# Kernel optimization log

Hardware: AMD Instinct MI355X
Metric: run time of the kernel (lower is better)

## Reference

```python
import jax, jax.numpy as jnp
import numpy as np

H = 16          # num query heads
G = 4           # num kv heads (groups)
MAX_POS = 128   # max relative position


def setup_inputs() -> dict:
    key = jax.random.key(0)
    ks = jax.random.split(key, 6)
    B, T, D = 8, 1024, 1024
    hd = D // H
    s = 0.02
    return {
        "x": jax.random.normal(ks[0], (B, T, D), jnp.float32),
        "Wq": jax.random.normal(ks[1], (D, D), jnp.float32) * s,
        "Wk": jax.random.normal(ks[2], (hd * G, D), jnp.float32) * s,
        "Wv": jax.random.normal(ks[3], (hd * G, D), jnp.float32) * s,
        "Wo": jax.random.normal(ks[4], (D, D), jnp.float32) * s,
        "E": jax.random.normal(ks[5], (2 * MAX_POS - 1, hd), jnp.float32) * s,
    }


def reference(x, Wq, Wk, Wv, Wo, E):
    B, T, D = x.shape
    hd = D // H
    r = H // G  # kv repeat factor

    # projections (torch nn.Linear convention: y = x @ W.T)
    q = (x @ Wq.T).reshape(B, T, H, hd).transpose(0, 2, 1, 3)  # [B,H,T,hd]
    k = (x @ Wk.T).reshape(B, T, G, hd)                         # [B,T,G,hd]
    v = (x @ Wv.T).reshape(B, T, G, hd)

    # GQA: query head h uses kv group h // r  (matches repeat_interleave)
    k = jnp.repeat(k, r, axis=2).transpose(0, 2, 1, 3)  # [B,H,T,hd]
    v = jnp.repeat(v, r, axis=2).transpose(0, 2, 1, 3)  # [B,H,T,hd]

    q = q * (1.0 / hd) ** 0.5
    scores = jnp.einsum("bhqd,bhkd->bhqk", q, k)  # [B,H,T,T]

    # relative position bias: R[i,j] = E[clamp(j - i) + MAX_POS - 1]
    pos = jnp.arange(T)
    dist = jnp.clip(pos[None, :] - pos[:, None], -MAX_POS + 1, MAX_POS - 1) + MAX_POS - 1
    R = E[dist]  # [T,T,hd]
    # original einsum 'bhd,thd->bht' with q=[B*H, Tq, hd], R=[Tk, Tq, hd]:
    # bias[b,h,q,kpos] = sum_d q[b,h,q,d] * R[kpos, q, d]
    bias = jnp.einsum("bhqd,kqd->bhqk", q, R)
    scores = scores + bias

    attn = jax.nn.softmax(scores, axis=-1)
    out = jnp.einsum("bhqk,bhkd->bhqd", attn, v)         # [B,H,T,hd]
    out = out.transpose(0, 2, 1, 3).reshape(B, T, D)      # [B,T,D]
    return out @ Wo.T
```

## Files before the change

kernel.cpp:

```cpp
#include <hip/hip_runtime.h>
#include <hip/hip_bf16.h>
#include <cstdint>
#include <cstddef>

typedef __hip_bfloat16 bf16;
typedef __attribute__((ext_vector_type(8))) __bf16 bf16x8;
typedef __attribute__((ext_vector_type(4))) float floatx4;

#define GPTR(p) ((const __attribute__((address_space(1))) void*)(p))
#define LPTR(p) ((__attribute__((address_space(3))) void*)(p))

extern "C" __device__ float __ocml_native_exp2_f32(float);
__device__ __forceinline__ float exp2n(float x) {
  return __ocml_native_exp2_f32(x);
}

__device__ __forceinline__ floatx4 mfma16(bf16x8 a, bf16x8 b, floatx4 c) {
  return __builtin_amdgcn_mfma_f32_16x16x32_bf16(a, b, c, 0, 0, 0);
}

__device__ __forceinline__ void cvt4(const float* __restrict__ in,
                                     bf16* __restrict__ out, int i) {
  float4 v = ((const float4*)in)[i];
  alignas(8) bf16 t[4] = {__float2bfloat16(v.x), __float2bfloat16(v.y),
                          __float2bfloat16(v.z), __float2bfloat16(v.w)};
  *(uint64_t*)(out + (size_t)i * 4) = *(const uint64_t*)t;
}

__global__ __launch_bounds__(256) void cvt_bf16(const float* __restrict__ in,
                                                bf16* __restrict__ out, int n4) {
  for (int i = blockIdx.x * 256 + threadIdx.x; i < n4; i += gridDim.x * 256) {
    cvt4(in, out, i);
  }
}

__global__ __launch_bounds__(256) void cvt_all(
    const float* __restrict__ x, const float* __restrict__ wq,
    const float* __restrict__ wk, const float* __restrict__ wv,
    const float* __restrict__ wo, bf16* __restrict__ ox,
    bf16* __restrict__ oq, bf16* __restrict__ ok, bf16* __restrict__ ov,
    bf16* __restrict__ owo) {
  const int bid = blockIdx.x;
  if (bid < 2048) {
    for (int i = bid * 256 + threadIdx.x; i < 2097152; i += 2048 * 256)
      cvt4(x, ox, i);
  } else if (bid < 3584) {
    int i = (bid - 2048) * 256 + threadIdx.x;
    if (i < 262144) {
      cvt4(wq, oq, i);
    } else if (i < 327680) {
      cvt4(wk, ok, i - 262144);
    } else {
      cvt4(wv, ov, i - 327680);
    }
  } else {
    cvt4(wo, owo, (bid - 3584) * 256 + threadIdx.x);
  }
}

__device__ __forceinline__ void stage128_swz(const bf16* __restrict__ g,
                                             int gstride,
                                             bf16* __restrict__ dst, int tid) {
#pragma unroll
  for (int s = 0; s < 4; ++s) {
    int f = s * 256 + tid;
    int r = f >> 3, cb = f & 7;
    int cbg = cb ^ (r & 7);
    __builtin_amdgcn_global_load_lds(GPTR(g + (size_t)r * gstride + cbg * 8),
                                     LPTR(dst + f * 8), 16, 0, 0);
  }
}

__device__ __forceinline__ bf16x8 rd128_swz(const bf16* __restrict__ tile,
                                            int row, int ci) {
  return *(const bf16x8*)&tile[row * 64 + ((ci ^ (row & 7)) * 8)];
}

__global__ __launch_bounds__(256) void gemm_qkv(
    const bf16* __restrict__ A, const bf16* __restrict__ Wq,
    const bf16* __restrict__ Wk, const bf16* __restrict__ Wv,
    bf16* __restrict__ qout, bf16* __restrict__ kout,
    bf16* __restrict__ vTout) {
  __shared__ alignas(16) bf16 As[128 * 64];
  __shared__ alignas(16) bf16 Bs[128 * 64];
  const int tid = threadIdx.x;
  const int lane = tid & 63;
  const int w = tid >> 6;
  const int wr = w >> 1, wc = w & 1;
  const int quad = lane >> 4, c = lane & 15;
  const int phys = blockIdx.y * 12 + blockIdx.x;
  const int ll = phys >> 3;
  const int m0 = ((phys & 7) * 8 + ll / 12) * 128;
  const int nb = ll % 12;

  int mode, nloc;
  const bf16* Wp;
  if (nb < 8) {
    mode = 1; Wp = Wq + (size_t)nb * 128 * 1024; nloc = nb * 128;
  } else if (nb < 10) {
    mode = 2; Wp = Wk + (size_t)(nb - 8) * 128 * 1024; nloc = (nb - 8) * 128;
  } else {
    mode = 3; Wp = Wv + (size_t)(nb - 10) * 128 * 1024; nloc = (nb - 10) * 128;
  }

  const bf16* pa = A + (size_t)m0 * 1024;
  const bf16* pb = Wp;

  floatx4 acc[4][4] = {};

  for (int kt = 0; kt < 16; ++kt) {
    if (kt) __syncthreads();
    stage128_swz(pa, 1024, As, tid);
    stage128_swz(pb, 1024, Bs, tid);
    pa += 64; pb += 64;
    __syncthreads();
#pragma unroll
    for (int kk = 0; kk < 2; ++kk) {
      bf16x8 af[4], bfr[4];
#pragma unroll
      for (int i = 0; i < 4; ++i)
        af[i] = rd128_swz(As, wr * 64 + i * 16 + c, kk * 4 + quad);
#pragma unroll
      for (int j = 0; j < 4; ++j)
        bfr[j] = rd128_swz(Bs, wc * 64 + j * 16 + c, kk * 4 + quad);
#pragma unroll
      for (int i = 0; i < 4; ++i)
#pragma unroll
        for (int j = 0; j < 4; ++j)
          acc[i][j] = mfma16(af[i], bfr[j], acc[i][j]);
    }
  }

  if (mode == 3) {
#pragma unroll
    for (int i = 0; i < 4; ++i)
#pragma unroll
      for (int j = 0; j < 4; ++j) {
        int m = m0 + wr * 64 + i * 16 + quad * 4;
        int n = nloc + wc * 64 + j * 16 + c;
        int b = m >> 10, t = m & 1023, g = n >> 6, d = n & 63;
        alignas(8) bf16 tmp[4];
#pragma unroll
        for (int r = 0; r < 4; ++r) tmp[r] = __float2bfloat16(acc[i][j][r]);
        *(uint64_t*)(vTout + (((size_t)(b * 4 + g)) * 64 + d) * 1024 + t) =
            *(const uint64_t*)tmp;
      }
    return;
  }

  const float scale = (mode == 1) ? 0.18033688f : 1.0f;
#pragma unroll
  for (int i = 0; i < 4; ++i)
#pragma unroll
    for (int j = 0; j < 4; ++j)
#pragma unroll
      for (int r = 0; r < 4; ++r) {
        int m = m0 + wr * 64 + i * 16 + quad * 4 + r;
        int n = nloc + wc * 64 + j * 16 + c;
        int b = m >> 10, t = m & 1023;
        bf16 v = __float2bfloat16(acc[i][j][r] * scale);
        if (mode == 1) {
          int h = n >> 6;
          qout[(((size_t)(b * 16 + h)) * 1024 + t) * 64 + (n & 63)] = v;
        } else {
          int g = n >> 6;
          kout[(((size_t)(b * 4 + g)) * 1024 + t) * 64 + (n & 63)] = v;
        }
      }
}

__global__ __launch_bounds__(256) void gemm_o(const bf16* __restrict__ A,
                                              const bf16* __restrict__ W,
                                              float* __restrict__ out) {
  __shared__ alignas(16) bf16 As[128 * 64];
  __shared__ alignas(16) bf16 Bs[128 * 64];
  const int tid = threadIdx.x;
  const int lane = tid & 63;
  const int w = tid >> 6;
  const int wr = w >> 1, wc = w & 1;
  const int quad = lane >> 4, c = lane & 15;
  const int phys = blockIdx.y * 8 + blockIdx.x;
  const int ll = phys >> 3;
  const int m0 = ((phys & 7) * 8 + (ll >> 3)) * 128;
  const int n0 = (ll & 7) * 128;

  const bf16* pa = A + (size_t)m0 * 1024;
  const bf16* pb = W + (size_t)n0 * 1024;

  floatx4 acc[4][4] = {};

  for (int kt = 0; kt < 16; ++kt) {
    if (kt) __syncthreads();
    stage128_swz(pa, 1024, As, tid);
    stage128_swz(pb, 1024, Bs, tid);
    pa += 64; pb += 64;
    __syncthreads();
#pragma unroll
    for (int kk = 0; kk < 2; ++kk) {
      bf16x8 af[4], bfr[4];
#pragma unroll
      for (int i = 0; i < 4; ++i)
        af[i] = rd128_swz(As, wr * 64 + i * 16 + c, kk * 4 + quad);
#pragma unroll
      for (int j = 0; j < 4; ++j)
        bfr[j] = rd128_swz(Bs, wc * 64 + j * 16 + c, kk * 4 + quad);
#pragma unroll
      for (int i = 0; i < 4; ++i)
#pragma unroll
        for (int j = 0; j < 4; ++j)
          acc[i][j] = mfma16(af[i], bfr[j], acc[i][j]);
    }
  }

#pragma unroll
  for (int i = 0; i < 4; ++i)
#pragma unroll
    for (int j = 0; j < 4; ++j)
#pragma unroll
      for (int r = 0; r < 4; ++r) {
        int m = m0 + wr * 64 + i * 16 + quad * 4 + r;
        int n = n0 + wc * 64 + j * 16 + c;
        out[(size_t)m * 1024 + n] = acc[i][j][r];
      }
}

__device__ __forceinline__ void stage_tile_swz(const bf16* __restrict__ g,
                                               int gstride, bf16* __restrict__ dst,
                                               int tid) {
#pragma unroll
  for (int s = 0; s < 2; ++s) {
    int f = s * 256 + tid;
    int r = f >> 3, cb = f & 7;
    int cbg = cb ^ (r & 7);
    __builtin_amdgcn_global_load_lds(GPTR(g + (size_t)r * gstride + cbg * 8),
                                     LPTR(dst + f * 8), 16, 0, 0);
  }
}

__device__ __forceinline__ bf16x8 read_frag_swz(const bf16* __restrict__ tile,
                                                int row, int cb) {
  return *(const bf16x8*)&tile[row * 64 + ((cb ^ (row & 7)) * 8)];
}

__global__ __launch_bounds__(256, 3) void attn_kernel(
    const bf16* __restrict__ q_ws, const bf16* __restrict__ k_ws,
    const bf16* __restrict__ vT, const float* __restrict__ E,
    bf16* __restrict__ out) {
  __shared__ alignas(16) bf16 qEl[64 * 264];
  __shared__ alignas(16) bf16 Ks[64 * 72];
  __shared__ alignas(16) bf16 Vs[64 * 64];
  const int tid = threadIdx.x;
  const int lane = tid & 63, w = tid >> 6;
  const int quad = lane >> 4, c = lane & 15;
  const int phys = blockIdx.y * 16 + blockIdx.x;
  const int logical = (phys & 7) * 256 + (phys >> 3);
  const int bh = logical >> 4;
  const int b = bh >> 4, h = bh & 15, g = h >> 2;
  const int qb = (logical & 15) * 64 + w * 16;

  const bf16* qrow = q_ws + ((size_t)bh * 1024 + qb + c) * 64;
  bf16x8 qf0 = *(const bf16x8*)(qrow + quad * 8);
  bf16x8 qf1 = *(const bf16x8*)(qrow + 32 + quad * 8);

  for (int jn = 0; jn < 16; ++jn) {
    int er = jn * 16 + c;
    er = er > 254 ? 254 : er;
    const float* Ep = E + (size_t)er * 64;
    float4 e0 = *(const float4*)(Ep + quad * 8);
    float4 e1 = *(const float4*)(Ep + quad * 8 + 4);
    float4 e2 = *(const float4*)(Ep + 32 + quad * 8);
    float4 e3 = *(const float4*)(Ep + 32 + quad * 8 + 4);
    alignas(16) bf16 t0b[8] = {
        __float2bfloat16(e0.x), __float2bfloat16(e0.y), __float2bfloat16(e0.z),
        __float2bfloat16(e0.w), __float2bfloat16(e1.x), __float2bfloat16(e1.y),
        __float2bfloat16(e1.z), __float2bfloat16(e1.w)};
    alignas(16) bf16 t1b[8] = {
        __float2bfloat16(e2.x), __float2bfloat16(e2.y), __float2bfloat16(e2.z),
        __float2bfloat16(e2.w), __float2bfloat16(e3.x), __float2bfloat16(e3.y),
        __float2bfloat16(e3.z), __float2bfloat16(e3.w)};
    floatx4 a = {};
    a = mfma16(qf0, *(const bf16x8*)t0b, a);
    a = mfma16(qf1, *(const bf16x8*)t1b, a);
#pragma unroll
    for (int r = 0; r < 4; ++r)
      qEl[(w * 16 + quad * 4 + r) * 264 + jn * 16 + c] = __float2bfloat16(a[r]);
  }
  __syncthreads();

  const bf16* rowE = qEl + (size_t)(w * 16 + c) * 264;
  bf16* rowP = Ks + (size_t)(w * 16 + c) * 72;
  float mrow = -1e30f, lpart = 0.f;
  floatx4 o[4] = {};
  const bf16* kbase = k_ws + (size_t)(b * 4 + g) * 1024 * 64;
  const bf16* vbase = vT + (size_t)(b * 4 + g) * 64 * 1024;
  const float blo = __bfloat162float(rowE[254]);
  const float bhi = __bfloat162float(rowE[0]);

  for (int t0 = 0; t0 < 1024; t0 += 64) {
    stage_tile_swz(kbase + (size_t)t0 * 64, 64, Ks, tid);
    stage_tile_swz(vbase + t0, 1024, Vs, tid);
    __syncthreads();
    floatx4 S[4];
    __builtin_amdgcn_s_setprio(1);
#pragma unroll
    for (int j = 0; j < 4; ++j) {
      bf16x8 kf0 = read_frag_swz(Ks, j * 16 + c, quad);
      bf16x8 kf1 = read_frag_swz(Ks, j * 16 + c, quad + 4);
      floatx4 z = {};
      z = mfma16(kf0, qf0, z);
      S[j] = mfma16(kf1, qf1, z);
    }
    __builtin_amdgcn_s_setprio(0);
    const int dlt0 = qb + c - t0;
    if (t0 <= qb - 190) {
#pragma unroll
      for (int j = 0; j < 4; ++j)
#pragma unroll
        for (int r = 0; r < 4; ++r) S[j][r] += blo;
    } else if (t0 >= qb + 142) {
#pragma unroll
      for (int j = 0; j < 4; ++j)
#pragma unroll
        for (int r = 0; r < 4; ++r) S[j][r] += bhi;
    } else {
#pragma unroll
      for (int j = 0; j < 4; ++j)
#pragma unroll
        for (int r = 0; r < 4; ++r) {
          int dlt = dlt0 - j * 16 - quad * 4 - r;
          dlt = dlt > 127 ? 127 : (dlt < -127 ? -127 : dlt);
          S[j][r] += __bfloat162float(rowE[dlt + 127]);
        }
    }
    float mx = S[0][0];
#pragma unroll
    for (int j = 0; j < 4; ++j)
#pragma unroll
      for (int r = 0; r < 4; ++r) mx = fmaxf(mx, S[j][r]);
    if (__ballot(mx > mrow + 11.5f)) {
      float fm = fmaxf(mx, __shfl_xor(mx, 16, 64));
      fm = fmaxf(fm, __shfl_xor(fm, 32, 64));
      float nm = fmaxf(mrow, fm);
      float alpha = exp2n(mrow - nm);
      float av[4];
#pragma unroll
      for (int r = 0; r < 4; ++r) av[r] = __shfl(alpha, quad * 4 + r, 64);
#pragma unroll
      for (int jj = 0; jj < 4; ++jj)
#pragma unroll
        for (int r = 0; r < 4; ++r) o[jj][r] *= av[r];
      lpart *= alpha;
      mrow = nm;
    }
    float rs = 0.f;
#pragma unroll
    for (int j = 0; j < 4; ++j)
#pragma unroll
      for (int r = 0; r < 4; ++r) {
        float p = exp2n(S[j][r] - mrow);
        S[j][r] = p;
        rs += p;
      }
    lpart += rs;
    __syncthreads();
#pragma unroll
    for (int j = 0; j < 4; ++j) {
      alignas(8) bf16 tmp[4];
#pragma unroll
      for (int r = 0; r < 4; ++r) tmp[r] = __float2bfloat16(S[j][r]);
      *(uint64_t*)(rowP + j * 16 + quad * 4) = *(const uint64_t*)tmp;
    }
    __threadfence_block();
    __builtin_amdgcn_wave_barrier();
    bf16x8 pf0 = *(const bf16x8*)(rowP + quad * 8);
    bf16x8 pf1 = *(const bf16x8*)(rowP + 32 + quad * 8);
    __builtin_amdgcn_s_setprio(1);
#pragma unroll
    for (int jj = 0; jj < 4; ++jj) {
      bf16x8 vf0 = read_frag_swz(Vs, jj * 16 + c, quad);
      bf16x8 vf1 = read_frag_swz(Vs, jj * 16 + c, quad + 4);
      o[jj] = mfma16(pf0, vf0, o[jj]);
      o[jj] = mfma16(pf1, vf1, o[jj]);
    }
    __builtin_amdgcn_s_setprio(0);
    __syncthreads();
  }

  float lsum = lpart + __shfl_xor(lpart, 16, 64);
  lsum += __shfl_xor(lsum, 32, 64);
  float linv = 1.0f / lsum;
  float li4[4];
#pragma unroll
  for (int r = 0; r < 4; ++r) li4[r] = __shfl(linv, quad * 4 + r, 64);
#pragma unroll
  for (int jj = 0; jj < 4; ++jj)
#pragma unroll
    for (int r = 0; r < 4; ++r) {
      int qi = qb + quad * 4 + r;
      out[(((size_t)b * 1024 + qi) * 16 + h) * 64 + jj * 16 + c] =
          __float2bfloat16(o[jj][r] * li4[r]);
    }
}

extern "C" void kernel_launch(void* const* d_in, const int* in_sizes, int n_in,
                              void* d_out, int out_size, void* d_ws,
                              size_t ws_size, hipStream_t stream) {
  const float* x = (const float*)d_in[0];
  const float* Wq = (const float*)d_in[1];
  const float* Wk = (const float*)d_in[2];
  const float* Wv = (const float*)d_in[3];
  const float* Wo = (const float*)d_in[4];
  const float* E = (const float*)d_in[5];

  char* ws = (char*)d_ws;
  bf16* q_ws = (bf16*)d_out;
  bf16* x_bf = (bf16*)((char*)d_out + (16ull << 20));
  bf16* k_ws = (bf16*)(ws);
  bf16* vT = (bf16*)(ws + (4ull << 20));
  bf16* attn = (bf16*)(ws + (8ull << 20));
  bf16* Wq_bf = (bf16*)(ws + (8ull << 20));
  bf16* Wk_bf = (bf16*)(ws + (10ull << 20));
  bf16* Wv_bf = (bf16*)(ws + (10ull << 20) + (512ull << 10));
  float* outp = (float*)d_out;

  const bool early_wo = ws_size >= (26ull << 20);
  bf16* Wo_bf = early_wo ? (bf16*)(ws + (24ull << 20)) : (bf16*)ws;

  cvt_all<<<early_wo ? 4608 : 3584, 256, 0, stream>>>(
      x, Wq, Wk, Wv, Wo, x_bf, Wq_bf, Wk_bf, Wv_bf, Wo_bf);
  gemm_qkv<<<dim3(12, 64), 256, 0, stream>>>(x_bf, Wq_bf, Wk_bf, Wv_bf,
                                             q_ws, k_ws, vT);
  attn_kernel<<<dim3(16, 128), 256, 0, stream>>>(q_ws, k_ws, vT, E, attn);
  if (!early_wo) cvt_bf16<<<1024, 256, 0, stream>>>(Wo, Wo_bf, 262144);
  gemm_o<<<dim3(8, 64), 256, 0, stream>>>(attn, Wo_bf, outp);
}
```

Baseline: 261.9 us.

## Double-buffer QKV and output GEMMs with 32-wide K tiles

Both projection GEMMs now use two 128x32 LDS buffer pairs instead of one 128x64 pair. The async global-to-LDS loads for the next K slice are issued before the MFMAs on the current slice, so memory latency overlaps compute. Each step ends with one waitcnt plus barrier instead of two syncthreads per K step. The trade-offs are twice as many loop iterations with less work each, and one wasted extra load that wraps back to k=0 on the final step.

```diff
diff --git a/kernel.cpp b/kernel.cpp
--- a/kernel.cpp
+++ b/kernel.cpp
@@ -58,22 +58,40 @@
   }
 }
 
-__device__ __forceinline__ void stage128_swz(const bf16* __restrict__ g,
-                                             int gstride,
-                                             bf16* __restrict__ dst, int tid) {
-#pragma unroll
-  for (int s = 0; s < 4; ++s) {
+__device__ __forceinline__ void stage32_swz(const bf16* __restrict__ g,
+                                            int gstride,
+                                            bf16* __restrict__ dst, int tid) {
+#pragma unroll
+  for (int s = 0; s < 2; ++s) {
     int f = s * 256 + tid;
-    int r = f >> 3, cb = f & 7;
-    int cbg = cb ^ (r & 7);
+    int r = f >> 2, cb = f & 3;
+    int cbg = cb ^ ((r >> 1) & 3);
     __builtin_amdgcn_global_load_lds(GPTR(g + (size_t)r * gstride + cbg * 8),
                                      LPTR(dst + f * 8), 16, 0, 0);
   }
 }
 
-__device__ __forceinline__ bf16x8 rd128_swz(const bf16* __restrict__ tile,
-                                            int row, int ci) {
-  return *(const bf16x8*)&tile[row * 64 + ((ci ^ (row & 7)) * 8)];
+__device__ __forceinline__ bf16x8 rd32_swz(const bf16* __restrict__ tile,
+                                           int row, int q) {
+  return *(const bf16x8*)&tile[row * 32 + ((q ^ ((row >> 1) & 3)) * 8)];
+}
+
+__device__ __forceinline__ void mma_tile32(const bf16* __restrict__ As,
+                                           const bf16* __restrict__ Bs,
+                                           int wr, int wc, int c, int quad,
+                                           floatx4 (&acc)[4][4]) {
+  bf16x8 af[4], bfr[4];
+#pragma unroll
+  for (int i = 0; i < 4; ++i)
+    af[i] = rd32_swz(As, wr * 64 + i * 16 + c, quad);
+#pragma unroll
+  for (int j = 0; j < 4; ++j)
+    bfr[j] = rd32_swz(Bs, wc * 64 + j * 16 + c, quad);
+#pragma unroll
+  for (int i = 0; i < 4; ++i)
+#pragma unroll
+    for (int j = 0; j < 4; ++j)
+      acc[i][j] = mfma16(af[i], bfr[j], acc[i][j]);
 }
 
 __global__ __launch_bounds__(256) void gemm_qkv(
@@ -81,8 +99,10 @@
     const bf16* __restrict__ Wk, const bf16* __restrict__ Wv,
     bf16* __restrict__ qout, bf16* __restrict__ kout,
     bf16* __restrict__ vTout) {
-  __shared__ alignas(16) bf16 As[128 * 64];
-  __shared__ alignas(16) bf16 Bs[128 * 64];
+  __shared__ alignas(16) bf16 Aa[128 * 32];
+  __shared__ alignas(16) bf16 Ba[128 * 32];
+  __shared__ alignas(16) bf16 Ac[128 * 32];
+  __shared__ alignas(16) bf16 Bc[128 * 32];
   const int tid = threadIdx.x;
   const int lane = tid & 63;
   const int w = tid >> 6;
@@ -103,32 +123,30 @@
     mode = 3; Wp = Wv + (size_t)(nb - 10) * 128 * 1024; nloc = (nb - 10) * 128;
   }
 
-  const bf16* pa = A + (size_t)m0 * 1024;
-  const bf16* pb = Wp;
+  const bf16* Abase = A + (size_t)m0 * 1024;
+  const bf16* Bbase = Wp;
 
   floatx4 acc[4][4] = {};
 
-  for (int kt = 0; kt < 16; ++kt) {
-    if (kt) __syncthreads();
-    stage128_swz(pa, 1024, As, tid);
-    stage128_swz(pb, 1024, Bs, tid);
-    pa += 64; pb += 64;
-    __syncthreads();
-#pragma unroll
-    for (int kk = 0; kk < 2; ++kk) {
-      bf16x8 af[4], bfr[4];
-#pragma unroll
-      for (int i = 0; i < 4; ++i)
-        af[i] = rd128_swz(As, wr * 64 + i * 16 + c, kk * 4 + quad);
-#pragma unroll
-      for (int j = 0; j < 4; ++j)
-        bfr[j] = rd128_swz(Bs, wc * 64 + j * 16 + c, kk * 4 + quad);
-#pragma unroll
-      for (int i = 0; i < 4; ++i)
-#pragma unroll
-        for (int j = 0; j < 4; ++j)
-          acc[i][j] = mfma16(af[i], bfr[j], acc[i][j]);
-    }
+  stage32_swz(Abase, 1024, Aa, tid);
+  stage32_swz(Bbase, 1024, Ba, tid);
+  asm volatile("s_waitcnt vmcnt(0)" ::: "memory");
+  __builtin_amdgcn_s_barrier();
+
+#pragma unroll 1
+  for (int i = 0; i < 16; ++i) {
+    const int k1 = ((2 * i + 1) * 32) & 1023;
+    stage32_swz(Abase + k1, 1024, Ac, tid);
+    stage32_swz(Bbase + k1, 1024, Bc, tid);
+    mma_tile32(Aa, Ba, wr, wc, c, quad, acc);
+    asm volatile("s_waitcnt vmcnt(0)" ::: "memory");
+    __builtin_amdgcn_s_barrier();
+    const int k2 = ((2 * i + 2) * 32) & 1023;
+    stage32_swz(Abase + k2, 1024, Aa, tid);
+    stage32_swz(Bbase + k2, 1024, Ba, tid);
+    mma_tile32(Ac, Bc, wr, wc, c, quad, acc);
+    asm volatile("s_waitcnt vmcnt(0)" ::: "memory");
+    __builtin_amdgcn_s_barrier();
   }
 
   if (mode == 3) {
@@ -172,8 +190,10 @@
 __global__ __launch_bounds__(256) void gemm_o(const bf16* __restrict__ A,
                                               const bf16* __restrict__ W,
                                               float* __restrict__ out) {
-  __shared__ alignas(16) bf16 As[128 * 64];
-  __shared__ alignas(16) bf16 Bs[128 * 64];
+  __shared__ alignas(16) bf16 Aa[128 * 32];
+  __shared__ alignas(16) bf16 Ba[128 * 32];
+  __shared__ alignas(16) bf16 Ac[128 * 32];
+  __shared__ alignas(16) bf16 Bc[128 * 32];
   const int tid = threadIdx.x;
   const int lane = tid & 63;
   const int w = tid >> 6;
@@ -184,32 +204,30 @@
   const int m0 = ((phys & 7) * 8 + (ll >> 3)) * 128;
   const int n0 = (ll & 7) * 128;
 
-  const bf16* pa = A + (size_t)m0 * 1024;
-  const bf16* pb = W + (size_t)n0 * 1024;
+  const bf16* Abase = A + (size_t)m0 * 1024;
+  const bf16* Bbase = W + (size_t)n0 * 1024;
 
   floatx4 acc[4][4] = {};
 
-  for (int kt = 0; kt < 16; ++kt) {
-    if (kt) __syncthreads();
-    stage128_swz(pa, 1024, As, tid);
-    stage128_swz(pb, 1024, Bs, tid);
-    pa += 64; pb += 64;
-    __syncthreads();
-#pragma unroll
-    for (int kk = 0; kk < 2; ++kk) {
-      bf16x8 af[4], bfr[4];
-#pragma unroll
-      for (int i = 0; i < 4; ++i)
-        af[i] = rd128_swz(As, wr * 64 + i * 16 + c, kk * 4 + quad);
-#pragma unroll
-      for (int j = 0; j < 4; ++j)
-        bfr[j] = rd128_swz(Bs, wc * 64 + j * 16 + c, kk * 4 + quad);
-#pragma unroll
-      for (int i = 0; i < 4; ++i)
-#pragma unroll
-        for (int j = 0; j < 4; ++j)
-          acc[i][j] = mfma16(af[i], bfr[j], acc[i][j]);
-    }
+  stage32_swz(Abase, 1024, Aa, tid);
+  stage32_swz(Bbase, 1024, Ba, tid);
+  asm volatile("s_waitcnt vmcnt(0)" ::: "memory");
+  __builtin_amdgcn_s_barrier();
+
+#pragma unroll 1
+  for (int i = 0; i < 16; ++i) {
+    const int k1 = ((2 * i + 1) * 32) & 1023;
+    stage32_swz(Abase + k1, 1024, Ac, tid);
+    stage32_swz(Bbase + k1, 1024, Bc, tid);
+    mma_tile32(Aa, Ba, wr, wc, c, quad, acc);
+    asm volatile("s_waitcnt vmcnt(0)" ::: "memory");
+    __builtin_amdgcn_s_barrier();
+    const int k2 = ((2 * i + 2) * 32) & 1023;
+    stage32_swz(Abase + k2, 1024, Aa, tid);
+    stage32_swz(Bbase + k2, 1024, Ba, tid);
+    mma_tile32(Ac, Bc, wr, wc, c, quad, acc);
+    asm volatile("s_waitcnt vmcnt(0)" ::: "memory");
+    __builtin_amdgcn_s_barrier();
   }
 
 #pragma unroll
```

New measurement: 277.5 us. 1.06x slower.
